# Kernel optimization log

Measured on AMD Instinct MI355X. Metric: run time of the kernel, lower is better.

Reference implementation:

```python
import jax, jax.numpy as jnp
import numpy as np

LIGAND_W = 1.0
SIDECHAIN_W = 0.5
LIGAND_DIST_W = 0.2
SIDECHAIN_DIST_W = 0.1
CUTOFF = 5.0
EPS = 1e-12


def _pdist(x):
    # x: [..., N, 3] -> (dist [..., N, N], sq [..., N, N]); safe sqrt for grads
    d = x[..., :, None, :] - x[..., None, :, :]
    sq = jnp.sum(d * d, axis=-1)
    return jnp.sqrt(jnp.maximum(sq, EPS)), sq


def _masked_dist_loss(pred, tgt, valid):
    # pred/tgt: [..., N, 3], valid: [..., N] float. Returns (per-group loss, has-any flag)
    pd, _ = _pdist(pred)
    td, tsq = _pdist(tgt)
    pair = valid[..., :, None] * valid[..., None, :]
    dmask = pair * (tsq > 0.0).astype(pred.dtype) * (td <= CUTOFF).astype(pred.dtype)
    num = jnp.sum(dmask * (pd - td) ** 2, axis=(-1, -2))
    den = jnp.sum(dmask, axis=(-1, -2))
    return num / jnp.maximum(den, 1.0), den > 0.0


def setup_inputs() -> dict:
    key = jax.random.key(0)
    k1, k2, k3, k4, k5, k6 = jax.random.split(key, 6)
    B, L, R, A = 64, 512, 1024, 14
    ligand_tgt = jax.random.normal(k2, (B, L, 3), dtype=jnp.float32) * 3.0
    ligand_pred = ligand_tgt + 0.5 * jax.random.normal(k1, (B, L, 3), dtype=jnp.float32)
    sidechain_tgt = jax.random.normal(k4, (B, R, A, 3), dtype=jnp.float32) * 2.0
    sidechain_pred = sidechain_tgt + 0.5 * jax.random.normal(k3, (B, R, A, 3), dtype=jnp.float32)
    ligand_mask = jax.random.bernoulli(k5, 0.9, (B, L))
    atom_mask = jax.random.bernoulli(k6, 0.7, (B, R, A))
    return {
        'ligand_pred': ligand_pred, 'ligand_tgt': ligand_tgt,
        'sidechain_pred': sidechain_pred, 'sidechain_tgt': sidechain_tgt,
        'ligand_mask': ligand_mask, 'atom_mask': atom_mask,
    }


def reference(ligand_pred, ligand_tgt, sidechain_pred, sidechain_tgt, ligand_mask, atom_mask):
    f = ligand_pred.dtype
    lm = ligand_mask.astype(f)              # [B, L]
    am = atom_mask.astype(f)                # [B, R, A]

    # --- ligand coord loss: per-batch mse (mean over valid atoms * 3), then mean over batches ---
    se = jnp.sum((ligand_pred - ligand_tgt) ** 2, axis=-1) * lm   # [B, L]
    lig_cnt = jnp.sum(lm, axis=-1)                                # [B]
    ligand_loss = jnp.mean(jnp.sum(se, axis=-1) / (3.0 * jnp.maximum(lig_cnt, 1.0)))

    # --- ligand distance-preservation loss ---
    lig_d, lig_has = _masked_dist_loss(ligand_pred, ligand_tgt, lm)  # [B], [B]
    ligand_dist_loss = jnp.sum(jnp.where(lig_has, lig_d, 0.0)) / jnp.maximum(jnp.sum(lig_has.astype(f)), 1.0)

    # --- sidechain coord loss: per-atom mse (mean over 3), mean over all valid atoms ---
    atom_mse = jnp.mean((sidechain_pred - sidechain_tgt) ** 2, axis=-1)  # [B, R, A]
    sc_cnt = jnp.sum(am)
    sidechain_loss = jnp.sum(atom_mse * am) / jnp.maximum(sc_cnt, 1.0)

    # --- sidechain distance-preservation loss: per-residue groups ---
    sc_d, sc_has = _masked_dist_loss(sidechain_pred, sidechain_tgt, am)  # [B, R]
    sidechain_dist_loss = jnp.sum(jnp.where(sc_has, sc_d, 0.0)) / jnp.maximum(jnp.sum(sc_has.astype(f)), 1.0)

    total = (LIGAND_W * ligand_loss
             + LIGAND_DIST_W * ligand_dist_loss
             + SIDECHAIN_W * sidechain_loss
             + SIDECHAIN_DIST_W * sidechain_dist_loss)
    return total
```

## Files before the change

### kernel.cpp

```cpp
#include <hip/hip_runtime.h>

#define CUTOFF 5.0f
#define FSQRT(x) __builtin_amdgcn_sqrtf(x)


#define NSC_BLK 256
#define NLIG_BLK 512
#define GRID (NSC_BLK + NLIG_BLK)

#define PAIR_EVAL(ti, pi, tjx, tjy, tjz, pjx, pjy, pjz, w, numv, denv)    \
  {                                                                       \
    float dx = (ti).x - (tjx), dy = (ti).y - (tjy), dz = (ti).z - (tjz);  \
    float tsq = dx * dx + dy * dy + dz * dz;                              \
    float td = FSQRT(tsq);                                                \
    float ww = (w);                                                       \
    ww = (td <= CUTOFF) ? ww : 0.f;                                       \
    float qx = (pi).x - (pjx), qy = (pi).y - (pjy), qz = (pi).z - (pjz);  \
    float pd = FSQRT(qx * qx + qy * qy + qz * qz);                        \
    float dd = pd - td;                                                   \
    numv += (ww * dd) * dd;                                               \
    denv += ww;                                                           \
  }

__global__ __launch_bounds__(256) void fused_kernel(
    const float* __restrict__ lig_pred, const float* __restrict__ lig_tgt,
    const int* __restrict__ lig_mask,
    const float* __restrict__ sc_pred, const float* __restrict__ sc_tgt,
    const int* __restrict__ sc_mask,
    float* __restrict__ ws) {
  const int tid = threadIdx.x;
  __shared__ float4 stage4[1344];
  __shared__ float red[4][4];

  if (blockIdx.x < NSC_BLK) {
    const int sb = blockIdx.x;
    const int rl = tid & 127;
    const int rh = tid >> 7;
    float ax[14], ay[14], az[14];
    float bx[14], by[14], bz[14];

    const float4* srcp = (const float4*)(sc_pred + (size_t)sb * 10752);
    const float4* srct = (const float4*)(sc_tgt + (size_t)sb * 10752);
#pragma unroll
    for (int h = 0; h < 2; h++) {
      if (h) __syncthreads();
      for (int k = tid; k < 1344; k += 256) stage4[k] = srcp[h * 1344 + k];
      __syncthreads();
      if (rh == h) {
        const float* s = ((const float*)stage4) + rl * 42;
#pragma unroll
        for (int a = 0; a < 14; a++) {
          ax[a] = s[3 * a]; ay[a] = s[3 * a + 1]; az[a] = s[3 * a + 2];
        }
      }
    }
#pragma unroll
    for (int h = 0; h < 2; h++) {
      __syncthreads();
      for (int k = tid; k < 1344; k += 256) stage4[k] = srct[h * 1344 + k];
      __syncthreads();
      if (rh == h) {
        const float* s = ((const float*)stage4) + rl * 42;
#pragma unroll
        for (int a = 0; a < 14; a++) {
          bx[a] = s[3 * a]; by[a] = s[3 * a + 1]; bz[a] = s[3 * a + 2];
        }
      }
    }

    const int2* mp2 = (const int2*)(sc_mask + ((size_t)sb * 256 + tid) * 14);
    float m[14];
#pragma unroll
    for (int k = 0; k < 7; k++) {
      int2 v = mp2[k];
      m[2 * k] = (v.x != 0) ? 1.f : 0.f;
      m[2 * k + 1] = (v.y != 0) ? 1.f : 0.f;
    }

    float mse = 0.f, am = 0.f;
#pragma unroll
    for (int a = 0; a < 14; a++) {
      float dx = ax[a] - bx[a], dy = ay[a] - by[a], dz = az[a] - bz[a];
      mse += m[a] * ((dx * dx + dy * dy + dz * dz) * (1.f / 3.f));
      am += m[a];
      bx[a] += (1.f - m[a]) * (30000.f * (float)(a + 1));
    }

    float num = 0.f, den = 0.f;
#pragma unroll
    for (int j = 1; j < 14; j++) {
#pragma unroll
      for (int i = 0; i < j; i++) {
        float dx = bx[i] - bx[j], dy = by[i] - by[j], dz = bz[i] - bz[j];
        float tsq = dx * dx + dy * dy + dz * dz;
        float td = FSQRT(tsq);
        float w = (td <= CUTOFF) ? 1.f : 0.f;
        float qx = ax[i] - ax[j], qy = ay[i] - ay[j], qz = az[i] - az[j];
        float pd = FSQRT(qx * qx + qy * qy + qz * qz);
        float d = pd - td;
        num += (w * d) * d;
        den += w;
      }
    }
    float val = (den > 0.f) ? (num + num) / fmaxf(den + den, 1.f) : 0.f;
    float has = (den > 0.f) ? 1.f : 0.f;

    for (int off = 32; off > 0; off >>= 1) {
      mse += __shfl_down(mse, off, 64);
      am += __shfl_down(am, off, 64);
      val += __shfl_down(val, off, 64);
      has += __shfl_down(has, off, 64);
    }
    int lane = tid & 63, wv = tid >> 6;
    if (lane == 0) { red[0][wv] = mse; red[1][wv] = am; red[2][wv] = val; red[3][wv] = has; }
    __syncthreads();
    if (tid == 0) {
      float* p = ws + 1088 + (size_t)sb * 4;
      p[0] = red[0][0] + red[0][1] + red[0][2] + red[0][3];
      p[1] = red[1][0] + red[1][1] + red[1][2] + red[1][3];
      p[2] = red[2][0] + red[2][1] + red[2][2] + red[2][3];
      p[3] = red[3][0] + red[3][1] + red[3][2] + red[3][3];
    }
  } else {
    const int L = 512;
    const int lb = blockIdx.x - NSC_BLK;
    const int b = lb >> 3;
    const int t = lb & 7;
    const int i0a = 32 * t;
    const int i0b = 32 * (15 - t);
    const float* pb = lig_pred + (size_t)b * L * 3;
    const float* tb = lig_tgt + (size_t)b * L * 3;
    const int* mb = lig_mask + (size_t)b * L;

    float4* st4 = stage4;
    float4* sp4 = stage4 + 64;

    if (tid < 128) {
      int which = tid >> 5;
      int idx = tid & 31;
      int i = ((which & 1) ? i0b : i0a) + idx;
      if (which < 2) {
        st4[(which << 5) + idx] =
            make_float4(tb[3 * i], tb[3 * i + 1], tb[3 * i + 2], (mb[i] != 0) ? 1.f : 0.f);
      } else {
        sp4[((which & 1) << 5) + idx] =
            make_float4(pb[3 * i], pb[3 * i + 1], pb[3 * i + 2], 0.f);
      }
    }

    const int jA0 = i0a + tid;
    const int jA1r = i0a + 256 + tid;
    const int jA1 = jA1r & (L - 1);
    const int jBr = i0b + tid;
    const int jB = jBr & (L - 1);

    float pA0x = pb[3 * jA0], pA0y = pb[3 * jA0 + 1], pA0z = pb[3 * jA0 + 2];
    float tA0x = tb[3 * jA0], tA0y = tb[3 * jA0 + 1], tA0z = tb[3 * jA0 + 2];
    float mA0 = (mb[jA0] != 0) ? 1.f : 0.f;
    float pA1x = pb[3 * jA1], pA1y = pb[3 * jA1 + 1], pA1z = pb[3 * jA1 + 2];
    float tA1x = tb[3 * jA1], tA1y = tb[3 * jA1 + 1], tA1z = tb[3 * jA1 + 2];
    float mA1 = (jA1r < L && mb[jA1] != 0) ? 1.f : 0.f;
    float pBx = pb[3 * jB], pBy = pb[3 * jB + 1], pBz = pb[3 * jB + 2];
    float tBx = tb[3 * jB], tBy = tb[3 * jB + 1], tBz = tb[3 * jB + 2];
    float mB = (jBr < L && mb[jB] != 0) ? 1.f : 0.f;

    float se = 0.f, cnt = 0.f;
    if (t == 0) {
      float dx = pA0x - tA0x, dy = pA0y - tA0y, dz = pA0z - tA0z;
      se += mA0 * (dx * dx + dy * dy + dz * dz);
      cnt += mA0;
      dx = pA1x - tA1x; dy = pA1y - tA1y; dz = pA1z - tA1z;
      se += mA1 * (dx * dx + dy * dy + dz * dz);
      cnt += mA1;
    }
    __syncthreads();

    float nA0 = 0.f, dA0 = 0.f, nA1 = 0.f, dA1 = 0.f, nB = 0.f, dB = 0.f;
#pragma unroll 8
    for (int ii = 0; ii < 32; ii++) {
      float4 tiA = st4[ii];
      float4 piA = sp4[ii];
      float4 tiB = st4[32 + ii];
      float4 piB = sp4[32 + ii];
      float wA0 = (tid > ii) ? tiA.w * mA0 : 0.f;
      PAIR_EVAL(tiA, piA, tA0x, tA0y, tA0z, pA0x, pA0y, pA0z, wA0, nA0, dA0);
      float wA1 = tiA.w * mA1;
      PAIR_EVAL(tiA, piA, tA1x, tA1y, tA1z, pA1x, pA1y, pA1z, wA1, nA1, dA1);
      float wB = (tid > ii) ? tiB.w * mB : 0.f;
      PAIR_EVAL(tiB, piB, tBx, tBy, tBz, pBx, pBy, pBz, wB, nB, dB);
    }

    float num = nA0 + nA1 + nB, den = dA0 + dA1 + dB;
    for (int off = 32; off > 0; off >>= 1) {
      num += __shfl_down(num, off, 64);
      den += __shfl_down(den, off, 64);
      se += __shfl_down(se, off, 64);
      cnt += __shfl_down(cnt, off, 64);
    }
    int lane = tid & 63, wv = tid >> 6;
    if (lane == 0) { red[0][wv] = num; red[1][wv] = den; red[2][wv] = se; red[3][wv] = cnt; }
    __syncthreads();
    if (tid == 0) {
      ws[lb * 2 + 0] = red[0][0] + red[0][1] + red[0][2] + red[0][3];
      ws[lb * 2 + 1] = red[1][0] + red[1][1] + red[1][2] + red[1][3];
      if (t == 0) {
        float se_t = red[2][0] + red[2][1] + red[2][2] + red[2][3];
        float cnt_t = red[3][0] + red[3][1] + red[3][2] + red[3][3];
        ws[1024 + b] = se_t / (3.f * fmaxf(cnt_t, 1.f));
      }
    }
  }
}

__global__ __launch_bounds__(256) void finalize_kernel(const float* __restrict__ ws,
                                                       float* __restrict__ out) {
  const int tid = threadIdx.x;
  __shared__ float sred[4][4];

  const float* sc = ws + 1088 + (size_t)tid * 4;
  float s0 = sc[0], s1 = sc[1], s2 = sc[2], s3 = sc[3];
  for (int off = 32; off > 0; off >>= 1) {
    s0 += __shfl_down(s0, off, 64);
    s1 += __shfl_down(s1, off, 64);
    s2 += __shfl_down(s2, off, 64);
    s3 += __shfl_down(s3, off, 64);
  }
  int lane = tid & 63, wv = tid >> 6;
  if (lane == 0) { sred[0][wv] = s0; sred[1][wv] = s1; sred[2][wv] = s2; sred[3][wv] = s3; }
  __syncthreads();

  float lval = 0.f, lhas = 0.f, lcoord = 0.f;
  if (tid < 64) {
    float n = 0.f, d = 0.f;
    for (int t = 0; t < 8; t++) {
      n += ws[(tid * 8 + t) * 2 + 0];
      d += ws[(tid * 8 + t) * 2 + 1];
    }
    lval = (d > 0.f) ? n / fmaxf(d, 1.f) : 0.f;
    lhas = (d > 0.f) ? 1.f : 0.f;
    lcoord = ws[1024 + tid];
    for (int off = 32; off > 0; off >>= 1) {
      lval += __shfl_down(lval, off, 64);
      lhas += __shfl_down(lhas, off, 64);
      lcoord += __shfl_down(lcoord, off, 64);
    }
  }
  if (tid == 0) {
    float sc_mse = sred[0][0] + sred[0][1] + sred[0][2] + sred[0][3];
    float sc_am = sred[1][0] + sred[1][1] + sred[1][2] + sred[1][3];
    float sc_val = sred[2][0] + sred[2][1] + sred[2][2] + sred[2][3];
    float sc_has = sred[3][0] + sred[3][1] + sred[3][2] + sred[3][3];
    float ligand_loss = lcoord * (1.f / 64.f);
    float ligand_dist_loss = lval / fmaxf(lhas, 1.f);
    float sidechain_loss = sc_mse / fmaxf(sc_am, 1.f);
    float sidechain_dist_loss = sc_val / fmaxf(sc_has, 1.f);
    out[0] = ligand_loss + 0.2f * ligand_dist_loss + 0.5f * sidechain_loss +
             0.1f * sidechain_dist_loss;
  }
}

extern "C" void kernel_launch(void* const* d_in, const int* in_sizes, int n_in,
                              void* d_out, int out_size, void* d_ws, size_t ws_size,
                              hipStream_t stream) {
  const float* ligand_pred = (const float*)d_in[0];
  const float* ligand_tgt = (const float*)d_in[1];
  const float* sidechain_pred = (const float*)d_in[2];
  const float* sidechain_tgt = (const float*)d_in[3];
  const int* ligand_mask = (const int*)d_in[4];
  const int* atom_mask = (const int*)d_in[5];
  float* out = (float*)d_out;
  float* ws = (float*)d_ws;

  fused_kernel<<<GRID, 256, 0, stream>>>(ligand_pred, ligand_tgt, ligand_mask,
                                         sidechain_pred, sidechain_tgt, atom_mask, ws);
  finalize_kernel<<<1, 256, 0, stream>>>(ws, out);
}
```

Baseline: 106.2 us.

## Split sidechain pair work across two threads per residue, doubling sidechain blocks

Each sidechain block now handles 128 residues instead of 256, and the 91 atom pairs of each residue are split between two threads (45 and 46 pairs). Partial sums are combined through shared memory. The intent is to double the thread-level parallelism and shorten per-thread latency in the sidechain path. The cost is extra blocks, a shared-memory exchange plus sync, duplicated register loads, and a finalize step that reduces twice as many partials.

```diff
diff --git a/kernel.cpp b/kernel.cpp
--- a/kernel.cpp
+++ b/kernel.cpp
@@ -4,7 +4,7 @@
 #define FSQRT(x) __builtin_amdgcn_sqrtf(x)
 
 
-#define NSC_BLK 256
+#define NSC_BLK 512
 #define NLIG_BLK 512
 #define GRID (NSC_BLK + NLIG_BLK)
 
@@ -31,44 +31,38 @@
   const int tid = threadIdx.x;
   __shared__ float4 stage4[1344];
   __shared__ float red[4][4];
+  __shared__ float2 scpart[128];
 
   if (blockIdx.x < NSC_BLK) {
     const int sb = blockIdx.x;
-    const int rl = tid & 127;
-    const int rh = tid >> 7;
+    const int r = tid & 127;
+    const int half = tid >> 7;
     float ax[14], ay[14], az[14];
     float bx[14], by[14], bz[14];
 
-    const float4* srcp = (const float4*)(sc_pred + (size_t)sb * 10752);
-    const float4* srct = (const float4*)(sc_tgt + (size_t)sb * 10752);
-#pragma unroll
-    for (int h = 0; h < 2; h++) {
-      if (h) __syncthreads();
-      for (int k = tid; k < 1344; k += 256) stage4[k] = srcp[h * 1344 + k];
-      __syncthreads();
-      if (rh == h) {
-        const float* s = ((const float*)stage4) + rl * 42;
-#pragma unroll
-        for (int a = 0; a < 14; a++) {
-          ax[a] = s[3 * a]; ay[a] = s[3 * a + 1]; az[a] = s[3 * a + 2];
-        }
-      }
-    }
-#pragma unroll
-    for (int h = 0; h < 2; h++) {
-      __syncthreads();
-      for (int k = tid; k < 1344; k += 256) stage4[k] = srct[h * 1344 + k];
-      __syncthreads();
-      if (rh == h) {
-        const float* s = ((const float*)stage4) + rl * 42;
-#pragma unroll
-        for (int a = 0; a < 14; a++) {
-          bx[a] = s[3 * a]; by[a] = s[3 * a + 1]; bz[a] = s[3 * a + 2];
-        }
-      }
-    }
-
-    const int2* mp2 = (const int2*)(sc_mask + ((size_t)sb * 256 + tid) * 14);
+    const float4* srcp = (const float4*)(sc_pred + (size_t)sb * 5376);
+    for (int k = tid; k < 1344; k += 256) stage4[k] = srcp[k];
+    __syncthreads();
+    {
+      const float* s = ((const float*)stage4) + r * 42;
+#pragma unroll
+      for (int a = 0; a < 14; a++) {
+        ax[a] = s[3 * a]; ay[a] = s[3 * a + 1]; az[a] = s[3 * a + 2];
+      }
+    }
+    __syncthreads();
+    const float4* srct = (const float4*)(sc_tgt + (size_t)sb * 5376);
+    for (int k = tid; k < 1344; k += 256) stage4[k] = srct[k];
+    __syncthreads();
+    {
+      const float* s = ((const float*)stage4) + r * 42;
+#pragma unroll
+      for (int a = 0; a < 14; a++) {
+        bx[a] = s[3 * a]; by[a] = s[3 * a + 1]; bz[a] = s[3 * a + 2];
+      }
+    }
+
+    const int2* mp2 = (const int2*)(sc_mask + (size_t)sb * 1792 + r * 14);
     float m[14];
 #pragma unroll
     for (int k = 0; k < 7; k++) {
@@ -85,25 +79,50 @@
       am += m[a];
       bx[a] += (1.f - m[a]) * (30000.f * (float)(a + 1));
     }
+    if (half) { mse = 0.f; am = 0.f; }
 
     float num = 0.f, den = 0.f;
-#pragma unroll
-    for (int j = 1; j < 14; j++) {
-#pragma unroll
-      for (int i = 0; i < j; i++) {
-        float dx = bx[i] - bx[j], dy = by[i] - by[j], dz = bz[i] - bz[j];
-        float tsq = dx * dx + dy * dy + dz * dz;
-        float td = FSQRT(tsq);
-        float w = (td <= CUTOFF) ? 1.f : 0.f;
-        float qx = ax[i] - ax[j], qy = ay[i] - ay[j], qz = az[i] - az[j];
-        float pd = FSQRT(qx * qx + qy * qy + qz * qz);
-        float d = pd - td;
-        num += (w * d) * d;
-        den += w;
-      }
-    }
-    float val = (den > 0.f) ? (num + num) / fmaxf(den + den, 1.f) : 0.f;
-    float has = (den > 0.f) ? 1.f : 0.f;
+    if (half == 0) {
+#pragma unroll
+      for (int j = 1; j <= 9; j++) {
+#pragma unroll
+        for (int i = 0; i < j; i++) {
+          float dx = bx[i] - bx[j], dy = by[i] - by[j], dz = bz[i] - bz[j];
+          float td = FSQRT(dx * dx + dy * dy + dz * dz);
+          float w = (td <= CUTOFF) ? 1.f : 0.f;
+          float qx = ax[i] - ax[j], qy = ay[i] - ay[j], qz = az[i] - az[j];
+          float pd = FSQRT(qx * qx + qy * qy + qz * qz);
+          float d = pd - td;
+          num += (w * d) * d;
+          den += w;
+        }
+      }
+    } else {
+#pragma unroll
+      for (int j = 10; j <= 13; j++) {
+#pragma unroll
+        for (int i = 0; i < j; i++) {
+          float dx = bx[i] - bx[j], dy = by[i] - by[j], dz = bz[i] - bz[j];
+          float td = FSQRT(dx * dx + dy * dy + dz * dz);
+          float w = (td <= CUTOFF) ? 1.f : 0.f;
+          float qx = ax[i] - ax[j], qy = ay[i] - ay[j], qz = az[i] - az[j];
+          float pd = FSQRT(qx * qx + qy * qy + qz * qz);
+          float d = pd - td;
+          num += (w * d) * d;
+          den += w;
+        }
+      }
+    }
+
+    if (half == 1) scpart[r] = make_float2(num, den);
+    __syncthreads();
+    float val = 0.f, has = 0.f;
+    if (half == 0) {
+      float2 o = scpart[r];
+      float ng = num + o.x, dg = den + o.y;
+      val = (dg > 0.f) ? (ng + ng) / fmaxf(dg + dg, 1.f) : 0.f;
+      has = (dg > 0.f) ? 1.f : 0.f;
+    }
 
     for (int off = 32; off > 0; off >>= 1) {
       mse += __shfl_down(mse, off, 64);
@@ -217,8 +236,11 @@
   const int tid = threadIdx.x;
   __shared__ float sred[4][4];
 
-  const float* sc = ws + 1088 + (size_t)tid * 4;
-  float s0 = sc[0], s1 = sc[1], s2 = sc[2], s3 = sc[3];
+  const float* sc = ws + 1088;
+  float s0 = 0.f, s1 = 0.f, s2 = 0.f, s3 = 0.f;
+  for (int i = tid; i < 512; i += 256) {
+    s0 += sc[4 * i + 0]; s1 += sc[4 * i + 1]; s2 += sc[4 * i + 2]; s3 += sc[4 * i + 3];
+  }
   for (int off = 32; off > 0; off >>= 1) {
     s0 += __shfl_down(s0, off, 64);
     s1 += __shfl_down(s1, off, 64);
```

After: 99.33 us. 1.07x faster.
